# Optimization experiments

Measured on AMD Instinct MI355X. Metric: run time of the kernel, lower is better.

Reference implementation:

```python
import jax, jax.numpy as jnp
import numpy as np

B, T, C, H = 4096, 32, 180, 6
HD = C // H  # 30
EPS = 1e-5

def _ln(x, g, b):
    mu = jnp.mean(x, axis=-1, keepdims=True)
    var = jnp.mean(jnp.square(x - mu), axis=-1, keepdims=True)
    return (x - mu) * jax.lax.rsqrt(var + EPS) * g + b

def setup_inputs() -> dict:
    key = jax.random.key(0)
    ks = jax.random.split(key, 12)
    s_in = 1.0 / np.sqrt(C)
    s_ff = 1.0 / np.sqrt(4 * C)
    return {
        "x": jax.random.normal(ks[0], (B, T, C), jnp.float32),
        "wq": jax.random.normal(ks[1], (H, C, HD), jnp.float32) * s_in,
        "wk": jax.random.normal(ks[2], (H, C, HD), jnp.float32) * s_in,
        "wv": jax.random.normal(ks[3], (H, C, HD), jnp.float32) * s_in,
        "g1": jnp.ones((C,), jnp.float32),
        "be1": jnp.zeros((C,), jnp.float32),
        "g2": jnp.ones((C,), jnp.float32),
        "be2": jnp.zeros((C,), jnp.float32),
        "w1": jax.random.normal(ks[4], (C, 4 * C), jnp.float32) * s_in,
        "b1": jnp.zeros((4 * C,), jnp.float32),
        "w2": jax.random.normal(ks[5], (4 * C, C), jnp.float32) * s_ff,
        "b2": jnp.zeros((C,), jnp.float32),
    }

def reference(x, wq, wk, wv, g1, be1, g2, be2, w1, b1, w2, b2):
    Bv, Tv, Cv = x.shape
    h = _ln(x, g1, be1)
    # batched multi-head QKV (replaces per-head Python loop)
    q = jnp.einsum('btc,hcd->bhtd', h, wq)
    k = jnp.einsum('btc,hcd->bhtd', h, wk)
    v = jnp.einsum('btc,hcd->bhtd', h, wv)
    scores = jnp.einsum('bhtd,bhsd->bhts', q, k) * (HD ** -0.5)
    mask = jnp.tril(jnp.ones((Tv, Tv), bool))
    scores = jnp.where(mask, scores, -jnp.inf)
    attn = jax.nn.softmax(scores, axis=-1)  # dropout off (eval)
    out = jnp.einsum('bhts,bhsd->bhtd', attn, v)
    out = jnp.transpose(out, (0, 2, 1, 3)).reshape(Bv, Tv, Cv)  # concat heads
    x = x + out
    h2 = _ln(x, g2, be2)
    mlp = jax.nn.relu(h2 @ w1 + b1) @ w2 + b2  # dropout off (eval)
    return x + mlp
```

## Files before the change

kernel.cpp:

```cpp
#include <hip/hip_runtime.h>

typedef __attribute__((ext_vector_type(8))) short short8;
typedef __attribute__((ext_vector_type(4))) float f32x4;
typedef unsigned short ushort_t;
typedef unsigned int u32;
typedef unsigned long long u64;

#define MFMA16(a,b,c) __builtin_amdgcn_mfma_f32_16x16x32_bf16((a),(b),(c),0,0,0)

__device__ __forceinline__ ushort_t f2bf(float f){
  union { float f; u32 u; } v; v.f = f;
  u32 r = v.u + 0x7fffu + ((v.u >> 16) & 1u);
  return (ushort_t)(r >> 16);
}
__device__ __forceinline__ float bf2f(ushort_t h){
  union { u32 u; float f; } v; v.u = ((u32)h) << 16; return v.f;
}
__device__ __forceinline__ u64 pack4(float a, float b, float c, float d){
  u32 p0 = (u32)f2bf(a) | ((u32)f2bf(b) << 16);
  u32 p1 = (u32)f2bf(c) | ((u32)f2bf(d) << 16);
  return (u64)p0 | ((u64)p1 << 32);
}
__device__ __forceinline__ void pin(short8 &v){ asm volatile("" : "+v"(v)); }

template<int CTRL>
__device__ __forceinline__ float dpp_add(float x){
  union { float f; int i; } a, b;
  a.f = x;
  b.i = __builtin_amdgcn_update_dpp(a.i, a.i, CTRL, 0xF, 0xF, false);
  return x + b.f;
}
__device__ __forceinline__ float red4_add(float x){
  x = dpp_add<0xB1>(x); x = dpp_add<0x4E>(x);
  return x;
}

#define WQKV_ELEMS (576*192)
#define W1T_ELEMS  (768*192)
#define W2T_ELEMS  (192*768)

#define SH 200
#define SS 40

__global__ void prep_weights(const float* __restrict__ wq, const float* __restrict__ wk,
                             const float* __restrict__ wv, const float* __restrict__ w1,
                             const float* __restrict__ w2, ushort_t* __restrict__ ws){
  ushort_t* wqkv = ws;
  ushort_t* w1t = ws + WQKV_ELEMS;
  ushort_t* w2t = w1t + W1T_ELEMS;
  int tid = blockIdx.x * blockDim.x + threadIdx.x;
  int stride = gridDim.x * blockDim.x;
  for (int i = tid; i < WQKV_ELEMS; i += stride){
    int k = i % 192; int row = i / 192;
    int d = row & 31; int m = (row >> 5) % 3; int h = row / 96;
    float v = 0.f;
    if (d < 30 && k < 180){
      const float* W = (m == 0) ? wq : ((m == 1) ? wk : wv);
      v = W[(h*180 + k)*30 + d];
    }
    wqkv[i] = f2bf(v);
  }
  for (int i = tid; i < W1T_ELEMS; i += stride){
    int c = i % 192; int n = i / 192;
    float v = (n < 720 && c < 180) ? w1[c*720 + n] : 0.f;
    w1t[i] = f2bf(v);
  }
  for (int i = tid; i < W2T_ELEMS; i += stride){
    int c4 = i % 768; int n = i / 768;
    float v = (n < 180 && c4 < 720) ? w2[c4*180 + n] : 0.f;
    w2t[i] = f2bf(v);
  }
}

__global__ __launch_bounds__(256, 2)
void block_kernel(const float* __restrict__ x,
                  const float* __restrict__ g1, const float* __restrict__ be1,
                  const float* __restrict__ g2, const float* __restrict__ be2,
                  const float* __restrict__ b1, const float* __restrict__ b2,
                  const ushort_t* __restrict__ wqkv, const ushort_t* __restrict__ w1t,
                  const ushort_t* __restrict__ w2t, float* __restrict__ out){
  __shared__ __align__(16) ushort_t W[64*SH];
  __shared__ __align__(16) ushort_t hn[64*SH];
  __shared__ __align__(16) ushort_t att[64*SH];

  int tid = threadIdx.x;
  int wave = tid >> 6, lane = tid & 63;
  int quad = lane >> 4, c16 = lane & 15;
  long base = (long)blockIdx.x * 11520;

  {
    int row = tid >> 2, sub = tid & 3;
    int c0 = sub*48;
    f32x4 xv[12];
    float s1 = 0.f, s2 = 0.f;
    #pragma unroll
    for (int gi = 0; gi < 12; gi++){
      int c = c0 + gi*4;
      if (c < 180) xv[gi] = *(const f32x4*)(x + base + (long)row*180 + c);
      else         xv[gi] = (f32x4)0.f;
      s1 += xv[gi].x + xv[gi].y + xv[gi].z + xv[gi].w;
      s2 += xv[gi].x*xv[gi].x + xv[gi].y*xv[gi].y + xv[gi].z*xv[gi].z + xv[gi].w*xv[gi].w;
    }
    s1 = red4_add(s1); s2 = red4_add(s2);
    float mu = s1 * (1.f/180.f);
    float rstd = rsqrtf(s2 * (1.f/180.f) - mu*mu + 1e-5f);
    #pragma unroll
    for (int gi = 0; gi < 12; gi++){
      int c = c0 + gi*4;
      if (c < 180){
        f32x4 gg = *(const f32x4*)(g1 + c);
        f32x4 bb = *(const f32x4*)(be1 + c);
        *(u64*)(hn + row*SH + c) = pack4((xv[gi].x - mu)*rstd*gg.x + bb.x,
                                         (xv[gi].y - mu)*rstd*gg.y + bb.y,
                                         (xv[gi].z - mu)*rstd*gg.z + bb.z,
                                         (xv[gi].w - mu)*rstd*gg.w + bb.w);
      } else {
        *(u64*)(hn + row*SH + c) = 0ull;
      }
    }
  }
  __syncthreads();

  {
    ushort_t* buf0 = W + wave*(2*32*SS);
    ushort_t* buf1 = buf0 + 32*SS;
    const float scl = 0.18257418583505537f;

    for (int jj = 0; jj < 3; jj++){
      int j = wave*3 + jj;
      int bb = (j >= 6) ? 1 : 0;
      int head = j - 6*bb;
      const ushort_t* wbase = wqkv + head*(96*192);

      f32x4 accq[2][2], acck[2][2], accv[2][2];
      #pragma unroll
      for (int i = 0; i < 2; i++)
        #pragma unroll
        for (int jx = 0; jx < 2; jx++){ accq[i][jx]=(f32x4)0.f; acck[i][jx]=(f32x4)0.f; accv[i][jx]=(f32x4)0.f; }

      short8 aqw[2][6], akw[2][6];
      #pragma unroll
      for (int mt = 0; mt < 2; mt++)
        #pragma unroll
        for (int kk = 0; kk < 6; kk++){
          aqw[mt][kk] = *(const short8*)(wbase + (      mt*16 + c16)*192 + kk*32 + quad*8);
          akw[mt][kk] = *(const short8*)(wbase + (32  + mt*16 + c16)*192 + kk*32 + quad*8);
          pin(aqw[mt][kk]); pin(akw[mt][kk]);
        }
      short8 avc[2], avn[2];
      #pragma unroll
      for (int mt = 0; mt < 2; mt++)
        avc[mt] = *(const short8*)(wbase + (64 + mt*16 + c16)*192 + quad*8);
      #pragma unroll
      for (int kk = 0; kk < 6; kk++){
        if (kk < 5){
          #pragma unroll
          for (int mt = 0; mt < 2; mt++)
            avn[mt] = *(const short8*)(wbase + (64 + mt*16 + c16)*192 + (kk+1)*32 + quad*8);
        }
        short8 hf[2];
        #pragma unroll
        for (int nt = 0; nt < 2; nt++)
          hf[nt] = *(const short8*)(hn + (bb*32 + nt*16 + c16)*SH + kk*32 + quad*8);
        #pragma unroll
        for (int mt = 0; mt < 2; mt++)
          #pragma unroll
          for (int nt = 0; nt < 2; nt++){
            accq[mt][nt] = MFMA16(aqw[mt][kk], hf[nt], accq[mt][nt]);
            acck[mt][nt] = MFMA16(akw[mt][kk], hf[nt], acck[mt][nt]);
            accv[mt][nt] = MFMA16(hf[mt], avc[nt], accv[mt][nt]);
          }
        if (kk < 5){
          #pragma unroll
          for (int mt = 0; mt < 2; mt++) avc[mt] = avn[mt];
        }
      }
      #pragma unroll
      for (int mt = 0; mt < 2; mt++)
        #pragma unroll
        for (int nt = 0; nt < 2; nt++){
          *(u64*)(buf0 + (nt*16 + c16)*SS + mt*16 + quad*4) =
            pack4(accq[mt][nt][0], accq[mt][nt][1], accq[mt][nt][2], accq[mt][nt][3]);
          *(u64*)(buf1 + (nt*16 + c16)*SS + mt*16 + quad*4) =
            pack4(acck[mt][nt][0], acck[mt][nt][1], acck[mt][nt][2], acck[mt][nt][3]);
        }
      f32x4 sacc[2][2];
      #pragma unroll
      for (int i = 0; i < 2; i++){ sacc[i][0]=(f32x4)0.f; sacc[i][1]=(f32x4)0.f; }
      short8 akf[2], bqf[2];
      #pragma unroll
      for (int mt = 0; mt < 2; mt++) akf[mt] = *(const short8*)(buf1 + (mt*16 + c16)*SS + quad*8);
      #pragma unroll
      for (int nt = 0; nt < 2; nt++) bqf[nt] = *(const short8*)(buf0 + (nt*16 + c16)*SS + quad*8);
      #pragma unroll
      for (int mt = 0; mt < 2; mt++)
        #pragma unroll
        for (int nt = 0; nt < 2; nt++)
          sacc[mt][nt] = MFMA16(akf[mt], bqf[nt], sacc[mt][nt]);
      #pragma unroll
      for (int nt = 0; nt < 2; nt++){
        int t = nt*16 + c16;
        float v[8];
        #pragma unroll
        for (int r = 0; r < 4; r++){
          int s0 = quad*4 + r, s1v = 16 + quad*4 + r;
          v[r]   = (s0  > t) ? -1e30f : sacc[0][nt][r]*scl;
          v[4+r] = (s1v > t) ? -1e30f : sacc[1][nt][r]*scl;
        }
        float m = v[0];
        #pragma unroll
        for (int i = 1; i < 8; i++) m = fmaxf(m, v[i]);
        m = fmaxf(m, __shfl_xor(m, 16));
        m = fmaxf(m, __shfl_xor(m, 32));
        float e[8], s = 0.f;
        #pragma unroll
        for (int i = 0; i < 8; i++){ e[i] = __expf(v[i] - m); s += e[i]; }
        s += __shfl_xor(s, 16);
        s += __shfl_xor(s, 32);
        float inv = 1.f / s;
        *(u64*)(buf1 + t*SS +      quad*4) = pack4(e[0]*inv, e[1]*inv, e[2]*inv, e[3]*inv);
        *(u64*)(buf1 + t*SS + 16 + quad*4) = pack4(e[4]*inv, e[5]*inv, e[6]*inv, e[7]*inv);
      }
      #pragma unroll
      for (int mt = 0; mt < 2; mt++)
        #pragma unroll
        for (int nt = 0; nt < 2; nt++)
          *(u64*)(buf0 + (nt*16 + c16)*SS + mt*16 + quad*4) =
            pack4(accv[mt][nt][0], accv[mt][nt][1], accv[mt][nt][2], accv[mt][nt][3]);
      f32x4 oacc[2][2];
      #pragma unroll
      for (int i = 0; i < 2; i++){ oacc[i][0]=(f32x4)0.f; oacc[i][1]=(f32x4)0.f; }
      short8 avf[2], bpf[2];
      #pragma unroll
      for (int mt = 0; mt < 2; mt++) avf[mt] = *(const short8*)(buf0 + (mt*16 + c16)*SS + quad*8);
      #pragma unroll
      for (int nt = 0; nt < 2; nt++) bpf[nt] = *(const short8*)(buf1 + (nt*16 + c16)*SS + quad*8);
      #pragma unroll
      for (int mt = 0; mt < 2; mt++)
        #pragma unroll
        for (int nt = 0; nt < 2; nt++){
          oacc[mt][nt] = MFMA16(avf[mt], bpf[nt], oacc[mt][nt]);
          *(u64*)(att + (bb*32 + nt*16 + c16)*SH + head*32 + mt*16 + quad*4) =
            pack4(oacc[mt][nt][0], oacc[mt][nt][1], oacc[mt][nt][2], oacc[mt][nt][3]);
        }
    }
  }
  __syncthreads();

  #pragma unroll
  for (int it = 0; it < 12; it++){
    int idx = it*256 + tid;
    if (idx < 2880){
      f32x4 v = *(const f32x4*)(x + base + (long)idx*4);
      int row = (int)(((u32)idx * 745655u) >> 25);
      int col4 = (idx - row*45)*4;
      #pragma unroll
      for (int e = 0; e < 4; e++){
        int c = col4 + e;
        int h = (c*4370) >> 17;
        int d = c - h*30;
        v[e] += bf2f(att[row*SH + h*32 + d]);
      }
      *(f32x4*)(out + base + (long)idx*4) = v;
      *(u64*)(hn + row*SH + col4) = pack4(v.x, v.y, v.z, v.w);
    } else {
      int p = idx - 2880;
      int row = (p*21846) >> 16;
      int g = p - row*3;
      *(u64*)(hn + row*SH + 180 + g*4) = 0ull;
    }
  }
  __syncthreads();

  {
    int row = tid >> 2, sub = tid & 3;
    int c0 = sub*48;
    float s1 = 0.f, s2 = 0.f;
    u64 mv[12];
    #pragma unroll
    for (int gi = 0; gi < 12; gi++){
      mv[gi] = *(const u64*)(hn + row*SH + c0 + gi*4);
      #pragma unroll
      for (int e = 0; e < 4; e++){
        float v = bf2f((ushort_t)(mv[gi] >> (16*e)));
        s1 += v; s2 += v*v;
      }
    }
    s1 = red4_add(s1); s2 = red4_add(s2);
    float mu = s1 * (1.f/180.f);
    float rstd = rsqrtf(s2 * (1.f/180.f) - mu*mu + 1e-5f);
    #pragma unroll
    for (int gi = 0; gi < 12; gi++){
      int c = c0 + gi*4;
      if (c < 180){
        f32x4 gg = *(const f32x4*)(g2 + c);
        f32x4 bb = *(const f32x4*)(be2 + c);
        float v0 = (bf2f((ushort_t)(mv[gi]    )) - mu)*rstd*gg.x + bb.x;
        float v1 = (bf2f((ushort_t)(mv[gi]>>16)) - mu)*rstd*gg.y + bb.y;
        float v2 = (bf2f((ushort_t)(mv[gi]>>32)) - mu)*rstd*gg.z + bb.z;
        float v3 = (bf2f((ushort_t)(mv[gi]>>48)) - mu)*rstd*gg.w + bb.w;
        *(u64*)(hn + row*SH + c) = pack4(v0, v1, v2, v3);
      }
    }
  }
  __syncthreads();

  {
    ushort_t* act = W;
    f32x4 outacc[4][3];
    #pragma unroll
    for (int i = 0; i < 4; i++)
      #pragma unroll
      for (int jx = 0; jx < 3; jx++) outacc[i][jx] = (f32x4)0.f;

    for (int ch = 0; ch < 4; ch++){
      f32x4 aacc[3][4];
      #pragma unroll
      for (int i = 0; i < 3; i++)
        #pragma unroll
        for (int jx = 0; jx < 4; jx++) aacc[i][jx] = (f32x4)0.f;
      short8 aw[3][6];
      #pragma unroll
      for (int mi = 0; mi < 3; mi++)
        #pragma unroll
        for (int kk = 0; kk < 6; kk++){
          aw[mi][kk] = *(const short8*)(w1t + (size_t)(ch*192 + (wave*3+mi)*16 + c16)*192 + kk*32 + quad*8);
          pin(aw[mi][kk]);
        }
      #pragma unroll
      for (int kk = 0; kk < 6; kk++){
        short8 bh[4];
        #pragma unroll
        for (int tt = 0; tt < 4; tt++)
          bh[tt] = *(const short8*)(hn + (tt*16 + c16)*SH + kk*32 + quad*8);
        #pragma unroll
        for (int mi = 0; mi < 3; mi++)
          #pragma unroll
          for (int tt = 0; tt < 4; tt++)
            aacc[mi][tt] = MFMA16(aw[mi][kk], bh[tt], aacc[mi][tt]);
      }
      __syncthreads();
      #pragma unroll
      for (int mi = 0; mi < 3; mi++){
        int nrel = (wave*3+mi)*16 + quad*4;
        int nabs = ch*192 + nrel;
        f32x4 bias = (f32x4)0.f;
        if (nabs < 720) bias = *(const f32x4*)(b1 + nabs);
        #pragma unroll
        for (int tt = 0; tt < 4; tt++){
          float v0 = fmaxf(aacc[mi][tt][0] + bias[0], 0.f);
          float v1 = fmaxf(aacc[mi][tt][1] + bias[1], 0.f);
          float v2 = fmaxf(aacc[mi][tt][2] + bias[2], 0.f);
          float v3 = fmaxf(aacc[mi][tt][3] + bias[3], 0.f);
          *(u64*)(act + (tt*16 + c16)*SH + nrel) = pack4(v0, v1, v2, v3);
        }
      }
      __syncthreads();
      short8 bw[3][6];
      #pragma unroll
      for (int ntl = 0; ntl < 3; ntl++)
        #pragma unroll
        for (int kk = 0; kk < 6; kk++){
          bw[ntl][kk] = *(const short8*)(w2t + (size_t)(wave*48 + ntl*16 + c16)*768 + ch*192 + kk*32 + quad*8);
          pin(bw[ntl][kk]);
        }
      #pragma unroll
      for (int kk = 0; kk < 6; kk++){
        short8 aa[4];
        #pragma unroll
        for (int tt = 0; tt < 4; tt++)
          aa[tt] = *(const short8*)(act + (tt*16 + c16)*SH + kk*32 + quad*8);
        #pragma unroll
        for (int tt = 0; tt < 4; tt++)
          #pragma unroll
          for (int ntl = 0; ntl < 3; ntl++)
            outacc[tt][ntl] = MFMA16(aa[tt], bw[ntl][kk], outacc[tt][ntl]);
      }
    }
    #pragma unroll
    for (int ntl = 0; ntl < 3; ntl++){
      int no = wave*48 + ntl*16 + c16;
      if (no < 180){
        float bias = b2[no];
        #pragma unroll
        for (int tt = 0; tt < 4; tt++){
          #pragma unroll
          for (int r = 0; r < 4; r++){
            long a = base + (long)(tt*16 + quad*4 + r)*180 + no;
            out[a] = out[a] + outacc[tt][ntl][r] + bias;
          }
        }
      }
    }
  }
}

extern "C" void kernel_launch(void* const* d_in, const int* in_sizes, int n_in,
                              void* d_out, int out_size, void* d_ws, size_t ws_size,
                              hipStream_t stream) {
  const float* x   = (const float*)d_in[0];
  const float* wq  = (const float*)d_in[1];
  const float* wk  = (const float*)d_in[2];
  const float* wv  = (const float*)d_in[3];
  const float* g1  = (const float*)d_in[4];
  const float* be1 = (const float*)d_in[5];
  const float* g2  = (const float*)d_in[6];
  const float* be2 = (const float*)d_in[7];
  const float* w1  = (const float*)d_in[8];
  const float* b1  = (const float*)d_in[9];
  const float* w2  = (const float*)d_in[10];
  const float* b2  = (const float*)d_in[11];
  ushort_t* ws   = (ushort_t*)d_ws;
  ushort_t* wqkv = ws;
  ushort_t* w1t  = ws + WQKV_ELEMS;
  ushort_t* w2t  = w1t + W1T_ELEMS;
  float* out = (float*)d_out;

  prep_weights<<<512, 256, 0, stream>>>(wq, wk, wv, w1, w2, ws);
  block_kernel<<<2048, 256, 0, stream>>>(x, g1, be1, g2, be2, b1, b2,
                                         wqkv, w1t, w2t, out);
}
```

Before: 503.3 us.

## Tile weight prep through LDS, compact attention buffer, add sched barriers

The weight-prep kernel now stages each weight slice in LDS so that both the global reads and the packed bf16 writes are coalesced, and it launches 42 blocks instead of 512. In the main kernel the attention output is written with a compact per-head stride of 30, so the residual-add pass can read four contiguous bf16 values with one 64-bit load instead of doing per-element head/dim index arithmetic. The x loads in the residual and LayerNorm sections are hoisted into register arrays, and sched_barrier calls are placed after weight-fragment loads to keep global loads issued early. The extra registers used for hoisted loads may reduce occupancy, and the prep kernel now runs on far fewer blocks.

Result: slower. 516.0 us (+2.5%).

```diff
diff --git a/kernel.cpp b/kernel.cpp
--- a/kernel.cpp
+++ b/kernel.cpp
@@ -7,6 +7,7 @@
 typedef unsigned long long u64;
 
 #define MFMA16(a,b,c) __builtin_amdgcn_mfma_f32_16x16x32_bf16((a),(b),(c),0,0,0)
+#define SBAR() __builtin_amdgcn_sched_barrier(0)
 
 __device__ __forceinline__ ushort_t f2bf(float f){
   union { float f; u32 u; } v; v.f = f;
@@ -20,6 +21,9 @@
   u32 p0 = (u32)f2bf(a) | ((u32)f2bf(b) << 16);
   u32 p1 = (u32)f2bf(c) | ((u32)f2bf(d) << 16);
   return (u64)p0 | ((u64)p1 << 32);
+}
+__device__ __forceinline__ u32 pack2(float a, float b){
+  return (u32)f2bf(a) | ((u32)f2bf(b) << 16);
 }
 __device__ __forceinline__ void pin(short8 &v){ asm volatile("" : "+v"(v)); }
 
@@ -41,34 +45,73 @@
 
 #define SH 200
 #define SS 40
+#define SA 184
 
 __global__ void prep_weights(const float* __restrict__ wq, const float* __restrict__ wk,
                              const float* __restrict__ wv, const float* __restrict__ w1,
                              const float* __restrict__ w2, ushort_t* __restrict__ ws){
+  __shared__ float lds_f[11700];
   ushort_t* wqkv = ws;
   ushort_t* w1t = ws + WQKV_ELEMS;
   ushort_t* w2t = w1t + W1T_ELEMS;
-  int tid = blockIdx.x * blockDim.x + threadIdx.x;
-  int stride = gridDim.x * blockDim.x;
-  for (int i = tid; i < WQKV_ELEMS; i += stride){
-    int k = i % 192; int row = i / 192;
-    int d = row & 31; int m = (row >> 5) % 3; int h = row / 96;
-    float v = 0.f;
-    if (d < 30 && k < 180){
-      const float* W = (m == 0) ? wq : ((m == 1) ? wk : wv);
-      v = W[(h*180 + k)*30 + d];
-    }
-    wqkv[i] = f2bf(v);
-  }
-  for (int i = tid; i < W1T_ELEMS; i += stride){
-    int c = i % 192; int n = i / 192;
-    float v = (n < 720 && c < 180) ? w1[c*720 + n] : 0.f;
-    w1t[i] = f2bf(v);
-  }
-  for (int i = tid; i < W2T_ELEMS; i += stride){
-    int c4 = i % 768; int n = i / 768;
-    float v = (n < 180 && c4 < 720) ? w2[c4*180 + n] : 0.f;
-    w2t[i] = f2bf(v);
+  int bid = blockIdx.x, tid = threadIdx.x;
+
+  if (bid < 18){
+    int h = bid / 3, m = bid % 3;
+    const float* src = ((m == 0) ? wq : (m == 1) ? wk : wv) + (size_t)h*180*30;
+    for (int l = 0; l < 22; l++){
+      int idx = tid + l*256;
+      if (idx < 5400) lds_f[idx] = src[idx];
+    }
+    __syncthreads();
+    u32* dst = (u32*)wqkv;
+    #pragma unroll
+    for (int l = 0; l < 12; l++){
+      int j = tid + l*256;
+      int d = j / 96, kp = j - d*96;
+      int k0 = 2*kp;
+      float f0 = (d < 30 && k0   < 180) ? lds_f[k0*30 + d]     : 0.f;
+      float f1 = (d < 30 && k0+1 < 180) ? lds_f[(k0+1)*30 + d] : 0.f;
+      dst[(size_t)(h*96 + m*32 + d)*96 + kp] = pack2(f0, f1);
+    }
+  } else if (bid < 30){
+    int n0 = (bid - 18) * 64;
+    #pragma unroll
+    for (int l = 0; l < 45; l++){
+      int idx = tid + l*256;
+      int c = idx >> 6, nl = idx & 63;
+      int n = n0 + nl;
+      lds_f[nl*180 + c] = (n < 720) ? w1[(size_t)c*720 + n] : 0.f;
+    }
+    __syncthreads();
+    u32* dst = (u32*)w1t;
+    #pragma unroll
+    for (int l = 0; l < 24; l++){
+      int j = tid + l*256;
+      int nl = j / 96, cp = j - nl*96;
+      int c0 = 2*cp;
+      float f0 = (c0   < 180) ? lds_f[nl*180 + c0]     : 0.f;
+      float f1 = (c0+1 < 180) ? lds_f[nl*180 + c0 + 1] : 0.f;
+      dst[(size_t)(n0 + nl)*96 + cp] = pack2(f0, f1);
+    }
+  } else {
+    int c40 = (bid - 30) * 64;
+    #pragma unroll
+    for (int l = 0; l < 45; l++){
+      int idx = tid + l*256;
+      int c4l = idx / 180, no = idx - c4l*180;
+      lds_f[no*65 + c4l] = (c40 + c4l < 720) ? w2[(size_t)(c40 + c4l)*180 + no] : 0.f;
+    }
+    __syncthreads();
+    u32* dst = (u32*)w2t;
+    #pragma unroll
+    for (int l = 0; l < 24; l++){
+      int j = tid + l*256;
+      int no = j >> 5, cp = j & 31;
+      float f0 = (no < 180) ? lds_f[no*65 + 2*cp]     : 0.f;
+      float f1 = (no < 180) ? lds_f[no*65 + 2*cp + 1] : 0.f;
+      dst[(size_t)no*384 + (c40 >> 1) + cp] = pack2(f0, f1);
+    }
   }
 }
 
@@ -81,7 +124,7 @@
                   const ushort_t* __restrict__ w2t, float* __restrict__ out){
   __shared__ __align__(16) ushort_t W[64*SH];
   __shared__ __align__(16) ushort_t hn[64*SH];
-  __shared__ __align__(16) ushort_t att[64*SH];
+  __shared__ __align__(16) ushort_t att[64*SA];
 
   int tid = threadIdx.x;
   int wave = tid >> 6, lane = tid & 63;
@@ -92,12 +135,16 @@
     int row = tid >> 2, sub = tid & 3;
     int c0 = sub*48;
     f32x4 xv[12];
-    float s1 = 0.f, s2 = 0.f;
     #pragma unroll
     for (int gi = 0; gi < 12; gi++){
       int c = c0 + gi*4;
       if (c < 180) xv[gi] = *(const f32x4*)(x + base + (long)row*180 + c);
       else         xv[gi] = (f32x4)0.f;
+    }
+    SBAR();
+    float s1 = 0.f, s2 = 0.f;
+    #pragma unroll
+    for (int gi = 0; gi < 12; gi++){
       s1 += xv[gi].x + xv[gi].y + xv[gi].z + xv[gi].w;
       s2 += xv[gi].x*xv[gi].x + xv[gi].y*xv[gi].y + xv[gi].z*xv[gi].z + xv[gi].w*xv[gi].w;
     }
@@ -147,6 +194,7 @@
           akw[mt][kk] = *(const short8*)(wbase + (32  + mt*16 + c16)*192 + kk*32 + quad*8);
           pin(aqw[mt][kk]); pin(akw[mt][kk]);
         }
+      SBAR();
       short8 avc[2], avn[2];
       #pragma unroll
       for (int mt = 0; mt < 2; mt++)
@@ -238,36 +286,51 @@
       #pragma unroll
       for (int mt = 0; mt < 2; mt++)
         #pragma unroll
+        for (int nt = 0; nt < 2; nt++)
+          oacc[mt][nt] = MFMA16(avf[mt], bpf[nt], oacc[mt][nt]);
+      #pragma unroll
+      for (int mt = 0; mt < 2; mt++)
+        #pragma unroll
         for (int nt = 0; nt < 2; nt++){
-          oacc[mt][nt] = MFMA16(avf[mt], bpf[nt], oacc[mt][nt]);
-          *(u64*)(att + (bb*32 + nt*16 + c16)*SH + head*32 + mt*16 + quad*4) =
-            pack4(oacc[mt][nt][0], oacc[mt][nt][1], oacc[mt][nt][2], oacc[mt][nt][3]);
+          int t = bb*32 + nt*16 + c16;
+          int c = head*30 + mt*16 + quad*4;
+          ushort_t* p = att + t*SA + c;
+          *(u32*)(p) = pack2(oacc[mt][nt][0], oacc[mt][nt][1]);
+          if (mt == 0 || quad < 3)
+            *(u32*)(p + 2) = pack2(oacc[mt][nt][2], oacc[mt][nt][3]);
         }
     }
   }
   __syncthreads();
 
-  #pragma unroll
-  for (int it = 0; it < 12; it++){
-    int idx = it*256 + tid;
-    if (idx < 2880){
-      f32x4 v = *(const f32x4*)(x + base + (long)idx*4);
-      int row = (int)(((u32)idx * 745655u) >> 25);
-      int col4 = (idx - row*45)*4;
-      #pragma unroll
-      for (int e = 0; e < 4; e++){
-        int c = col4 + e;
-        int h = (c*4370) >> 17;
-        int d = c - h*30;
-        v[e] += bf2f(att[row*SH + h*32 + d]);
-      }
-      *(f32x4*)(out + base + (long)idx*4) = v;
-      *(u64*)(hn + row*SH + col4) = pack4(v.x, v.y, v.z, v.w);
-    } else {
-      int p = idx - 2880;
-      int row = (p*21846) >> 16;
-      int g = p - row*3;
-      *(u64*)(hn + row*SH + 180 + g*4) = 0ull;
+  {
+    f32x4 xv2[12];
+    #pragma unroll
+    for (int it = 0; it < 12; it++){
+      int idx = it*256 + tid;
+      if (idx < 2880) xv2[it] = *(const f32x4*)(x + base + (long)idx*4);
+    }
+    SBAR();
+    #pragma unroll
+    for (int it = 0; it < 12; it++){
+      int idx = it*256 + tid;
+      if (idx < 2880){
+        f32x4 v = xv2[it];
+        int row = (int)(((u32)idx * 745655u) >> 25);
+        int col4 = (idx - row*45)*4;
+        u64 m = *(const u64*)(att + row*SA + col4);
+        v.x += bf2f((ushort_t)(m      ));
+        v.y += bf2f((ushort_t)(m >> 16));
+        v.z += bf2f((ushort_t)(m >> 32));
+        v.w += bf2f((ushort_t)(m >> 48));
+        *(f32x4*)(out + base + (long)idx*4) = v;
+        *(u64*)(hn + row*SH + col4) = pack4(v.x, v.y, v.z, v.w);
+      } else {
+        int p = idx - 2880;
+        int row = (p*21846) >> 16;
+        int g = p - row*3;
+        *(u64*)(hn + row*SH + 180 + g*4) = 0ull;
+      }
     }
   }
   __syncthreads();
@@ -327,6 +390,7 @@
           aw[mi][kk] = *(const short8*)(w1t + (size_t)(ch*192 + (wave*3+mi)*16 + c16)*192 + kk*32 + quad*8);
           pin(aw[mi][kk]);
         }
+      SBAR();
       #pragma unroll
       for (int kk = 0; kk < 6; kk++){
         short8 bh[4];
@@ -364,6 +428,7 @@
           bw[ntl][kk] = *(const short8*)(w2t + (size_t)(wave*48 + ntl*16 + c16)*768 + ch*192 + kk*32 + quad*8);
           pin(bw[ntl][kk]);
         }
+      SBAR();
       #pragma unroll
       for (int kk = 0; kk < 6; kk++){
         short8 aa[4];
@@ -416,7 +481,7 @@
   ushort_t* w2t  = w1t + W1T_ELEMS;
   float* out = (float*)d_out;
 
-  prep_weights<<<512, 256, 0, stream>>>(wq, wk, wv, w1, w2, ws);
+  prep_weights<<<42, 256, 0, stream>>>(wq, wk, wv, w1, w2, ws);
   block_kernel<<<2048, 256, 0, stream>>>(x, g1, be1, g2, be2, b1, b2,
                                          wqkv, w1t, w2t, out);
 }
```
